# Optimization experiments

Hardware: AMD Instinct MI355X
Metric: run time of the kernel (lower is better)

## Reference

```python
import jax, jax.numpy as jnp
import numpy as np

DIM = 1024
HIDDEN = 4096
NUM_EXPERTS = 8
TOP_K = 2
B, S = 4, 2048


def setup_inputs() -> dict:
    key = jax.random.key(0)
    ks = jax.random.split(key, 5)
    scale_in = 1.0 / np.sqrt(DIM)
    scale_h = 1.0 / np.sqrt(HIDDEN)
    x = jax.random.normal(ks[0], (B, S, DIM), dtype=jnp.float32)
    gate_w = jax.random.normal(ks[1], (DIM, NUM_EXPERTS), dtype=jnp.float32) * scale_in
    w1 = jax.random.normal(ks[2], (NUM_EXPERTS, DIM, HIDDEN), dtype=jnp.float32) * scale_in
    w3 = jax.random.normal(ks[3], (NUM_EXPERTS, DIM, HIDDEN), dtype=jnp.float32) * scale_in
    w2 = jax.random.normal(ks[4], (NUM_EXPERTS, HIDDEN, DIM), dtype=jnp.float32) * scale_h
    return {"x": x, "gate_w": gate_w, "w1": w1, "w2": w2, "w3": w3}


def reference(x, gate_w, w1, w2, w3):
    b, s, d = x.shape
    e = w1.shape[0]
    k = TOP_K
    # --- Router ---
    gate_scores = jnp.einsum('bsd,de->bse', x, gate_w)           # [B,S,E]
    topk_vals, topk_idx = jax.lax.top_k(gate_scores, k)          # [B,S,K]
    topk_w = jax.nn.softmax(topk_vals, axis=-1)                  # [B,S,K]
    usage = jax.nn.softmax(gate_scores, axis=-1).mean(axis=(0, 1))  # [E]
    aux_loss = e * jnp.sum(usage ** 2)
    # --- Dispatch/combine weights: combine[t, e] = sum_k w where idx==e ---
    xf = x.reshape(-1, d)                                        # [T,D]
    idx_f = topk_idx.reshape(-1, k)                              # [T,K]
    w_f = topk_w.reshape(-1, k)                                  # [T,K]
    combine = jnp.sum(jax.nn.one_hot(idx_f, e, dtype=x.dtype) * w_f[..., None], axis=1)  # [T,E]
    # --- Per-expert SwiGLU, weighted combine (loop over fixed small E) ---
    out = jnp.zeros_like(xf)
    for ei in range(e):
        h = jax.nn.silu(xf @ w1[ei]) * (xf @ w3[ei])             # [T,H]
        y = h @ w2[ei]                                           # [T,D]
        out = out + combine[:, ei:ei + 1] * y
    return out.reshape(b, s, d), aux_loss
```

## Files before the change

### kernel.cpp

```cpp
#include <hip/hip_runtime.h>
#include <hip/hip_bf16.h>

#define NT 8192
#define DIM_ 1024
#define HID_ 4096
#define NE 8

#define TM 128
#define TN 128
#define BK 32

typedef unsigned short u16;
typedef __attribute__((ext_vector_type(8))) short bf16x8;
typedef __attribute__((ext_vector_type(4))) float f32x4;

__device__ __forceinline__ u16 f2b(float f) {
  unsigned u = __float_as_uint(f);
  return (u16)((u + 0x7FFFu + ((u >> 16) & 1u)) >> 16);
}

typedef __attribute__((address_space(1))) const unsigned int ga_u32;
typedef __attribute__((address_space(3))) unsigned int lds_u32;
__device__ __forceinline__ void gl16(const u16* g, u16* l) {
  __builtin_amdgcn_global_load_lds((ga_u32*)g, (lds_u32*)l, 16, 0, 0);
}

__global__ __launch_bounds__(256) void cvt_x_kernel(const float* __restrict__ x,
                                                    u16* __restrict__ xb) {
  int i = (blockIdx.x * 256 + threadIdx.x) * 4;
  f32x4 v = *(const f32x4*)(x + i);
  ushort4 o;
  o.x = f2b(v.x); o.y = f2b(v.y); o.z = f2b(v.z); o.w = f2b(v.w);
  *(ushort4*)(xb + i) = o;
}

__global__ __launch_bounds__(256) void tpose_kernel(const float* __restrict__ src,
                                                    u16* __restrict__ dst, int K, int N) {
  int e = blockIdx.z;
  int n0 = blockIdx.x * 64, k0 = blockIdx.y * 64;
  __shared__ u16 t[64][72];
  int tid = threadIdx.x;
  int kl = tid >> 4, cl = (tid & 15) * 4;
  const float* s = src + ((size_t)e * K + k0) * N + n0;
#pragma unroll
  for (int i = 0; i < 4; i++) {
    f32x4 v = *(const f32x4*)(s + (size_t)(kl + i * 16) * N + cl);
    ushort4 o; o.x = f2b(v.x); o.y = f2b(v.y); o.z = f2b(v.z); o.w = f2b(v.w);
    *(ushort4*)&t[kl + i * 16][cl] = o;
  }
  __syncthreads();
  int nl = tid >> 2, kc = (tid & 3) * 16;
  u16* d = dst + ((size_t)e * N + n0 + nl) * K + k0 + kc;
  unsigned p[8];
#pragma unroll
  for (int j = 0; j < 8; j++)
    p[j] = (unsigned)t[kc + 2 * j][nl] | ((unsigned)t[kc + 2 * j + 1][nl] << 16);
  *(uint4*)d = make_uint4(p[0], p[1], p[2], p[3]);
  *(uint4*)(d + 8) = make_uint4(p[4], p[5], p[6], p[7]);
}

__global__ __launch_bounds__(256) void router_kernel(
    const float* __restrict__ x, const float* __restrict__ gw,
    int* __restrict__ elist, float* __restrict__ pw,
    int* __restrict__ count, float* __restrict__ usage) {
  __shared__ float us[NE];
  int tid = threadIdx.x;
  if (tid < NE) us[tid] = 0.f;
  __syncthreads();
  int wave = tid >> 6, lane = tid & 63;
  int base = (blockIdx.x * 4 + wave) * 16;
  for (int i = 0; i < 16; ++i) {
    int t = base + i;
    float acc[NE];
#pragma unroll
    for (int e = 0; e < NE; e++) acc[e] = 0.f;
    for (int d = lane; d < DIM_; d += 64) {
      float xv = x[t * DIM_ + d];
      const float* g = gw + d * NE;
#pragma unroll
      for (int e = 0; e < NE; e++) acc[e] += xv * g[e];
    }
#pragma unroll
    for (int off = 32; off; off >>= 1) {
#pragma unroll
      for (int e = 0; e < NE; e++) acc[e] += __shfl_xor(acc[e], off);
    }
    if (lane == 0) {
      float m = acc[0];
#pragma unroll
      for (int e = 1; e < NE; e++) m = fmaxf(m, acc[e]);
      float Z = 0.f, ex[NE];
#pragma unroll
      for (int e = 0; e < NE; e++) { ex[e] = __expf(acc[e] - m); Z += ex[e]; }
#pragma unroll
      for (int e = 0; e < NE; e++) atomicAdd(&us[e], ex[e] / Z);
      int i0 = 0;
#pragma unroll
      for (int e = 1; e < NE; e++) if (acc[e] > acc[i0]) i0 = e;
      int i1 = -1;
#pragma unroll
      for (int e = 0; e < NE; e++) {
        if (e == i0) continue;
        if (i1 < 0 || acc[e] > acc[i1]) i1 = e;
      }
      float w0 = 1.f / (1.f + __expf(acc[i1] - acc[i0]));
      float w1 = 1.f - w0;
      int p0 = atomicAdd(&count[i0], 1);
      elist[i0 * NT + p0] = 2 * t;
      pw[2 * t] = w0;
      int p1 = atomicAdd(&count[i1], 1);
      elist[i1 * NT + p1] = 2 * t + 1;
      pw[2 * t + 1] = w1;
    }
  }
  __syncthreads();
  if (tid < NE) atomicAdd(&usage[tid], us[tid]);
}

__global__ void aux_kernel(const float* __restrict__ usage, float* __restrict__ out_aux) {
  if (threadIdx.x == 0) {
    float s = 0.f;
    for (int e = 0; e < NE; e++) { float u = usage[e] / (float)NT; s += u * u; }
    *out_aux = (float)NE * s;
  }
}

__global__ __launch_bounds__(256) void stage1_kernel(
    const u16* __restrict__ xb, const u16* __restrict__ wt1, const u16* __restrict__ wt3,
    const int* __restrict__ elist, const int* __restrict__ count,
    const float* __restrict__ pw, u16* __restrict__ hbuf) {
  int wgid = blockIdx.x;
  int e = wgid & 7;
  int k = wgid >> 3;
  int tile = k & 63;
  int n0 = (k >> 6) * TN;
  int cnt = count[e];
  if (tile * TM >= cnt) return;

  __shared__ u16 As[2][TM * BK];
  __shared__ u16 B1s[2][TN * BK];
  __shared__ u16 B3s[2][TN * BK];
  __shared__ int slots[TM];
  __shared__ float pws[TM];

  int tid = threadIdx.x;
  if (tid < TM) {
    int r = tile * TM + tid;
    int s = (r < cnt) ? elist[e * NT + r] : -1;
    slots[tid] = s;
    pws[tid] = (s >= 0) ? pw[s] : 0.f;
  }
  __syncthreads();

  int lrow = tid >> 2;
  int lcol = (tid & 3) * 8;
  int sl0 = slots[lrow], sl1 = slots[lrow + 64];
  const u16* gA0 = xb + (size_t)((sl0 >= 0 ? sl0 : 0) >> 1) * DIM_ + lcol;
  const u16* gA1 = xb + (size_t)((sl1 >= 0 ? sl1 : 0) >> 1) * DIM_ + lcol;
  const u16* gB1a = wt1 + ((size_t)e * HID_ + n0 + lrow) * DIM_ + lcol;
  const u16* gB1b = gB1a + (size_t)64 * DIM_;
  const u16* gB3a = wt3 + ((size_t)e * HID_ + n0 + lrow) * DIM_ + lcol;
  const u16* gB3b = gB3a + (size_t)64 * DIM_;

  int wv = tid >> 6, lane = tid & 63;
  int wm = (wv & 1) * 64, wn = (wv >> 1) * 64;
  int fr = lane & 15, fk = (lane >> 4) * 8;

  f32x4 acc1[4][4], acc3[4][4];
  f32x4 zero = {0.f, 0.f, 0.f, 0.f};
#pragma unroll
  for (int i = 0; i < 4; i++)
#pragma unroll
    for (int j = 0; j < 4; j++) { acc1[i][j] = zero; acc3[i][j] = zero; }

#define S1_STAGE(B, K0)                          \
  gl16(gA0 + (K0), &As[B][tid * 8]);             \
  gl16(gA1 + (K0), &As[B][2048 + tid * 8]);      \
  gl16(gB1a + (K0), &B1s[B][tid * 8]);           \
  gl16(gB1b + (K0), &B1s[B][2048 + tid * 8]);    \
  gl16(gB3a + (K0), &B3s[B][tid * 8]);           \
  gl16(gB3b + (K0), &B3s[B][2048 + tid * 8]);

#define S1_COMPUTE(B)                                                          \
  { bf16x8 afr[4], b1fr[4], b3fr[4];                                           \
    _Pragma("unroll") for (int i = 0; i < 4; i++)                              \
      afr[i] = *(const bf16x8*)&As[B][(wm + i * 16 + fr) * BK + fk];           \
    _Pragma("unroll") for (int j = 0; j < 4; j++) {                            \
      b1fr[j] = *(const bf16x8*)&B1s[B][(wn + j * 16 + fr) * BK + fk];         \
      b3fr[j] = *(const bf16x8*)&B3s[B][(wn + j * 16 + fr) * BK + fk];         \
    }                                                                          \
    _Pragma("unroll") for (int i = 0; i < 4; i++)                              \
      _Pragma("unroll") for (int j = 0; j < 4; j++) {                          \
        acc1[i][j] = __builtin_amdgcn_mfma_f32_16x16x32_bf16(afr[i], b1fr[j], acc1[i][j], 0, 0, 0); \
        acc3[i][j] = __builtin_amdgcn_mfma_f32_16x16x32_bf16(afr[i], b3fr[j], acc3[i][j], 0, 0, 0); \
      } }

  S1_STAGE(0, 0);
  __syncthreads();
  for (int k0 = 0; k0 < DIM_; k0 += 2 * BK) {
    S1_STAGE(1, k0 + BK);
    S1_COMPUTE(0);
    __syncthreads();
    if (k0 + 2 * BK < DIM_) { S1_STAGE(0, k0 + 2 * BK); }
    S1_COMPUTE(1);
    __syncthreads();
  }

#pragma unroll
  for (int i = 0; i < 4; i++) {
#pragma unroll
    for (int r4 = 0; r4 < 4; r4++) {
      int row = wm + i * 16 + (lane >> 4) * 4 + r4;
      int s = slots[row];
      if (s < 0) continue;
      float w = pws[row];
      u16* dst = hbuf + (size_t)s * HID_ + n0 + wn + (lane & 15);
#pragma unroll
      for (int j = 0; j < 4; j++) {
        float p1 = acc1[i][j][r4];
        float p3 = acc3[i][j][r4];
        float h = (p1 / (1.f + __expf(-p1))) * p3 * w;
        dst[j * 16] = f2b(h);
      }
    }
  }
}

__global__ __launch_bounds__(256) void stage2_kernel(
    const u16* __restrict__ hbuf, const u16* __restrict__ wt2,
    const int* __restrict__ elist, const int* __restrict__ count,
    float* __restrict__ out) {
  int wgid = blockIdx.x;
  int e = wgid & 7;
  int k = wgid >> 3;
  int tile = k & 63;
  int n0 = (k >> 6) * TN;
  int cnt = count[e];
  if (tile * TM >= cnt) return;

  __shared__ u16 As[2][TM * BK];
  __shared__ u16 Bs[2][TN * BK];
  __shared__ int slots[TM];

  int tid = threadIdx.x;
  if (tid < TM) {
    int r = tile * TM + tid;
    slots[tid] = (r < cnt) ? elist[e * NT + r] : -1;
  }
  __syncthreads();

  int lrow = tid >> 2;
  int lcol = (tid & 3) * 8;
  int sl0 = slots[lrow], sl1 = slots[lrow + 64];
  const u16* gA0 = hbuf + (size_t)(sl0 >= 0 ? sl0 : 0) * HID_ + lcol;
  const u16* gA1 = hbuf + (size_t)(sl1 >= 0 ? sl1 : 0) * HID_ + lcol;
  const u16* gBa = wt2 + ((size_t)e * DIM_ + n0 + lrow) * HID_ + lcol;
  const u16* gBb = gBa + (size_t)64 * HID_;

  int wv = tid >> 6, lane = tid & 63;
  int wm = (wv & 1) * 64, wn = (wv >> 1) * 64;
  int fr = lane & 15, fk = (lane >> 4) * 8;

  f32x4 acc[4][4];
  f32x4 zero = {0.f, 0.f, 0.f, 0.f};
#pragma unroll
  for (int i = 0; i < 4; i++)
#pragma unroll
    for (int j = 0; j < 4; j++) acc[i][j] = zero;

#define S2_STAGE(B, K0)                          \
  gl16(gA0 + (K0), &As[B][tid * 8]);             \
  gl16(gA1 + (K0), &As[B][2048 + tid * 8]);      \
  gl16(gBa + (K0), &Bs[B][tid * 8]);             \
  gl16(gBb + (K0), &Bs[B][2048 + tid * 8]);

#define S2_COMPUTE(B)                                                          \
  { bf16x8 afr[4], bfr[4];                                                     \
    _Pragma("unroll") for (int i = 0; i < 4; i++)                              \
      afr[i] = *(const bf16x8*)&As[B][(wm + i * 16 + fr) * BK + fk];           \
    _Pragma("unroll") for (int j = 0; j < 4; j++)                              \
      bfr[j] = *(const bf16x8*)&Bs[B][(wn + j * 16 + fr) * BK + fk];           \
    _Pragma("unroll") for (int i = 0; i < 4; i++)                              \
      _Pragma("unroll") for (int j = 0; j < 4; j++)                            \
        acc[i][j] = __builtin_amdgcn_mfma_f32_16x16x32_bf16(afr[i], bfr[j], acc[i][j], 0, 0, 0); }

  S2_STAGE(0, 0);
  __syncthreads();
  for (int k0 = 0; k0 < HID_; k0 += 2 * BK) {
    S2_STAGE(1, k0 + BK);
    S2_COMPUTE(0);
    __syncthreads();
    if (k0 + 2 * BK < HID_) { S2_STAGE(0, k0 + 2 * BK); }
    S2_COMPUTE(1);
    __syncthreads();
  }

#pragma unroll
  for (int i = 0; i < 4; i++) {
#pragma unroll
    for (int r4 = 0; r4 < 4; r4++) {
      int row = wm + i * 16 + (lane >> 4) * 4 + r4;
      int s = slots[row];
      if (s < 0) continue;
      int tk = s >> 1;
      float* dst = out + (size_t)tk * DIM_ + n0 + wn + (lane & 15);
#pragma unroll
      for (int j = 0; j < 4; j++) atomicAdd(&dst[j * 16], acc[i][j][r4]);
    }
  }
}

extern "C" void kernel_launch(void* const* d_in, const int* in_sizes, int n_in,
                              void* d_out, int out_size, void* d_ws, size_t ws_size,
                              hipStream_t stream) {
  const float* x = (const float*)d_in[0];
  const float* gw = (const float*)d_in[1];
  const float* w1 = (const float*)d_in[2];
  const float* w2 = (const float*)d_in[3];
  const float* w3 = (const float*)d_in[4];
  float* out = (float*)d_out;

  char* ws = (char*)d_ws;
  int* count = (int*)ws;
  float* usage = (float*)(ws + 32);
  int* elist = (int*)(ws + 256);
  float* pw = (float*)(ws + 256 + 262144);
  u16* xb = (u16*)(ws + 327936);
  u16* hbuf = (u16*)(ws + 327936 + 16777216);
  char* wbase = ws + 327936 + 16777216 + 134217728;
  u16* wt1 = (u16*)wbase;
  u16* wt3 = (u16*)(wbase + 67108864);
  u16* wt2 = (u16*)wbase;

  hipMemsetAsync(d_out, 0, (size_t)(NT * DIM_ + 1) * sizeof(float), stream);
  hipMemsetAsync(ws, 0, 64, stream);

  cvt_x_kernel<<<(NT * DIM_) / (256 * 4), 256, 0, stream>>>(x, xb);
  router_kernel<<<128, 256, 0, stream>>>(x, gw, elist, pw, count, usage);
  aux_kernel<<<1, 64, 0, stream>>>(usage, out + (size_t)NT * DIM_);
  tpose_kernel<<<dim3(HID_ / 64, DIM_ / 64, NE), 256, 0, stream>>>(w1, wt1, DIM_, HID_);
  tpose_kernel<<<dim3(HID_ / 64, DIM_ / 64, NE), 256, 0, stream>>>(w3, wt3, DIM_, HID_);
  stage1_kernel<<<dim3(NE * 64 * (HID_ / TN)), 256, 0, stream>>>(xb, wt1, wt3, elist, count, pw, hbuf);
  tpose_kernel<<<dim3(DIM_ / 64, HID_ / 64, NE), 256, 0, stream>>>(w2, wt2, HID_, DIM_);
  stage2_kernel<<<dim3(NE * 64 * (DIM_ / TN)), 256, 0, stream>>>(hbuf, wt2, elist, count, out);
}
```

Measured before the change: 1.604 ms.

## Triple-buffer LDS staging with vmcnt-based waits and one barrier per K step

Both GEMM stages move from a double-buffered loop with two __syncthreads per pair of K tiles to a three-stage ring of LDS buffers. Two tiles are kept in flight, and partial s_waitcnt vmcnt counts wait only for the oldest tile's global-to-LDS loads before a single barrier per step. The intent is deeper prefetch that hides global load latency and fewer full drains of outstanding memory operations. The cost is 50% more LDS per workgroup, which may lower occupancy. Correctness also depends on the hand-counted vmcnt values matching the number of loads issued per stage.

```diff
diff --git a/kernel.cpp b/kernel.cpp
--- a/kernel.cpp
+++ b/kernel.cpp
@@ -137,9 +137,9 @@
   int cnt = count[e];
   if (tile * TM >= cnt) return;
 
-  __shared__ u16 As[2][TM * BK];
-  __shared__ u16 B1s[2][TN * BK];
-  __shared__ u16 B3s[2][TN * BK];
+  __shared__ u16 As[3][TM * BK];
+  __shared__ u16 B1s[3][TN * BK];
+  __shared__ u16 B3s[3][TN * BK];
   __shared__ int slots[TM];
   __shared__ float pws[TM];
 
@@ -196,14 +196,22 @@
       } }
 
   S1_STAGE(0, 0);
-  __syncthreads();
-  for (int k0 = 0; k0 < DIM_; k0 += 2 * BK) {
-    S1_STAGE(1, k0 + BK);
-    S1_COMPUTE(0);
-    __syncthreads();
-    if (k0 + 2 * BK < DIM_) { S1_STAGE(0, k0 + 2 * BK); }
-    S1_COMPUTE(1);
-    __syncthreads();
+  S1_STAGE(1, BK);
+  int b0 = 0;
+  for (int k0 = 0; k0 < DIM_; k0 += BK) {
+    if (k0 + BK < DIM_) {
+      asm volatile("s_waitcnt vmcnt(6)" ::: "memory");
+    } else {
+      asm volatile("s_waitcnt vmcnt(0)" ::: "memory");
+    }
+    __builtin_amdgcn_s_barrier();
+    __builtin_amdgcn_sched_barrier(0);
+    if (k0 + 2 * BK < DIM_) {
+      int b2 = b0 + 2; if (b2 >= 3) b2 -= 3;
+      S1_STAGE(b2, k0 + 2 * BK);
+    }
+    S1_COMPUTE(b0);
+    if (++b0 == 3) b0 = 0;
   }
 
 #pragma unroll
@@ -238,8 +246,8 @@
   int cnt = count[e];
   if (tile * TM >= cnt) return;
 
-  __shared__ u16 As[2][TM * BK];
-  __shared__ u16 Bs[2][TN * BK];
+  __shared__ u16 As[3][TM * BK];
+  __shared__ u16 Bs[3][TN * BK];
   __shared__ int slots[TM];
 
   int tid = threadIdx.x;
@@ -285,14 +293,22 @@
         acc[i][j] = __builtin_amdgcn_mfma_f32_16x16x32_bf16(afr[i], bfr[j], acc[i][j], 0, 0, 0); }
 
   S2_STAGE(0, 0);
-  __syncthreads();
-  for (int k0 = 0; k0 < HID_; k0 += 2 * BK) {
-    S2_STAGE(1, k0 + BK);
-    S2_COMPUTE(0);
-    __syncthreads();
-    if (k0 + 2 * BK < HID_) { S2_STAGE(0, k0 + 2 * BK); }
-    S2_COMPUTE(1);
-    __syncthreads();
+  S2_STAGE(1, BK);
+  int b0 = 0;
+  for (int k0 = 0; k0 < HID_; k0 += BK) {
+    if (k0 + BK < HID_) {
+      asm volatile("s_waitcnt vmcnt(4)" ::: "memory");
+    } else {
+      asm volatile("s_waitcnt vmcnt(0)" ::: "memory");
+    }
+    __builtin_amdgcn_s_barrier();
+    __builtin_amdgcn_sched_barrier(0);
+    if (k0 + 2 * BK < HID_) {
+      int b2 = b0 + 2; if (b2 >= 3) b2 -= 3;
+      S2_STAGE(b2, k0 + 2 * BK);
+    }
+    S2_COMPUTE(b0);
+    if (++b0 == 3) b0 = 0;
   }
 
 #pragma unroll
```

After: 1.668 ms. 1.04x slower.

## Restructure stage1 GEMM into 256x128 tiles with swizzled LDS and interleaved pipeline

Applied to the files above, without the earlier changes.

Stage1 moves to 512 threads with 256-row, 64-deep K tiles and an XOR-swizzled LDS layout to avoid bank conflicts. The main loop is split into four sub-phases with explicit barriers, waitcnt and setprio, so global-to-LDS loads of the next buffer overlap MFMA work. The goal is more data reuse per tile and better hiding of memory latency. The cost is much larger LDS use and fragile hand-written synchronisation. The grid still covers 64 tiles per expert even though each tile now holds 256 rows, so many blocks exit early.

```diff
diff --git a/kernel.cpp b/kernel.cpp
--- a/kernel.cpp
+++ b/kernel.cpp
@@ -9,6 +9,10 @@
 #define TM 128
 #define TN 128
 #define BK 32
+
+#define TM1 256
+#define TN1 128
+#define BK1 64
 
 typedef unsigned short u16;
 typedef __attribute__((ext_vector_type(8))) short bf16x8;
@@ -125,7 +129,7 @@
   }
 }
 
-__global__ __launch_bounds__(256) void stage1_kernel(
+__global__ __launch_bounds__(512, 2) void stage1_kernel(
     const u16* __restrict__ xb, const u16* __restrict__ wt1, const u16* __restrict__ wt3,
     const int* __restrict__ elist, const int* __restrict__ count,
     const float* __restrict__ pw, u16* __restrict__ hbuf) {
@@ -133,38 +137,60 @@
   int e = wgid & 7;
   int k = wgid >> 3;
   int tile = k & 63;
-  int n0 = (k >> 6) * TN;
+  int n0 = (k >> 6) * TN1;
   int cnt = count[e];
-  if (tile * TM >= cnt) return;
-
-  __shared__ u16 As[2][TM * BK];
-  __shared__ u16 B1s[2][TN * BK];
-  __shared__ u16 B3s[2][TN * BK];
-  __shared__ int slots[TM];
-  __shared__ float pws[TM];
+  if (tile * TM1 >= cnt) return;
+
+  __shared__ u16 As[2][TM1 * BK1];
+  __shared__ u16 B1s[2][TN1 * BK1];
+  __shared__ u16 B3s[2][TN1 * BK1];
+  __shared__ int slots[TM1];
+  __shared__ float pws[TM1];
 
   int tid = threadIdx.x;
-  if (tid < TM) {
-    int r = tile * TM + tid;
+  if (tid < TM1) {
+    int r = tile * TM1 + tid;
     int s = (r < cnt) ? elist[e * NT + r] : -1;
     slots[tid] = s;
     pws[tid] = (s >= 0) ? pw[s] : 0.f;
   }
   __syncthreads();
 
-  int lrow = tid >> 2;
-  int lcol = (tid & 3) * 8;
-  int sl0 = slots[lrow], sl1 = slots[lrow + 64];
-  const u16* gA0 = xb + (size_t)((sl0 >= 0 ? sl0 : 0) >> 1) * DIM_ + lcol;
-  const u16* gA1 = xb + (size_t)((sl1 >= 0 ? sl1 : 0) >> 1) * DIM_ + lcol;
-  const u16* gB1a = wt1 + ((size_t)e * HID_ + n0 + lrow) * DIM_ + lcol;
-  const u16* gB1b = gB1a + (size_t)64 * DIM_;
-  const u16* gB3a = wt3 + ((size_t)e * HID_ + n0 + lrow) * DIM_ + lcol;
-  const u16* gB3b = gB3a + (size_t)64 * DIM_;
+  int srow = tid >> 3;
+  int scol = ((tid & 7) ^ (srow & 7)) * 8;
+  const u16* gA[2][2];
+#pragma unroll
+  for (int h = 0; h < 2; h++)
+#pragma unroll
+    for (int r = 0; r < 2; r++) {
+      int rr = h * 128 + r * 64 + srow;
+      int s = slots[rr];
+      gA[h][r] = xb + (size_t)((s >= 0 ? s : 0) >> 1) * DIM_ + scol;
+    }
+  const u16* gB1r0 = wt1 + ((size_t)e * HID_ + n0 + srow) * DIM_ + scol;
+  const u16* gB1r1 = gB1r0 + (size_t)64 * DIM_;
+  const u16* gB3r0 = wt3 + ((size_t)e * HID_ + n0 + srow) * DIM_ + scol;
+  const u16* gB3r1 = gB3r0 + (size_t)64 * DIM_;
+
+#define STG_A(BUF, H, K0)                                   \
+  gl16(gA[H][0] + (K0), &As[BUF][(H) * 8192 + tid * 8]);    \
+  gl16(gA[H][1] + (K0), &As[BUF][(H) * 8192 + 4096 + tid * 8]);
+#define STG_B1(BUF, K0)                                     \
+  gl16(gB1r0 + (K0), &B1s[BUF][tid * 8]);                   \
+  gl16(gB1r1 + (K0), &B1s[BUF][4096 + tid * 8]);
+#define STG_B3(BUF, K0)                                     \
+  gl16(gB3r0 + (K0), &B3s[BUF][tid * 8]);                   \
+  gl16(gB3r1 + (K0), &B3s[BUF][4096 + tid * 8]);
 
   int wv = tid >> 6, lane = tid & 63;
-  int wm = (wv & 1) * 64, wn = (wv >> 1) * 64;
-  int fr = lane & 15, fk = (lane >> 4) * 8;
+  int wm = (wv & 3) * 64;
+  int wn = (wv >> 2) * 64;
+  int fr = lane & 15, q = lane >> 4;
+  int sw = fr & 7;
+  int aof0 = (wm + fr) * 64 + ((q ^ sw)) * 8;
+  int aof1 = (wm + fr) * 64 + (((4 + q) ^ sw)) * 8;
+  int bof0 = (wn + fr) * 64 + ((q ^ sw)) * 8;
+  int bof1 = (wn + fr) * 64 + (((4 + q) ^ sw)) * 8;
 
   f32x4 acc1[4][4], acc3[4][4];
   f32x4 zero = {0.f, 0.f, 0.f, 0.f};
@@ -173,38 +199,67 @@
 #pragma unroll
     for (int j = 0; j < 4; j++) { acc1[i][j] = zero; acc3[i][j] = zero; }
 
-#define S1_STAGE(B, K0)                          \
-  gl16(gA0 + (K0), &As[B][tid * 8]);             \
-  gl16(gA1 + (K0), &As[B][2048 + tid * 8]);      \
-  gl16(gB1a + (K0), &B1s[B][tid * 8]);           \
-  gl16(gB1b + (K0), &B1s[B][2048 + tid * 8]);    \
-  gl16(gB3a + (K0), &B3s[B][tid * 8]);           \
-  gl16(gB3b + (K0), &B3s[B][2048 + tid * 8]);
-
-#define S1_COMPUTE(B)                                                          \
-  { bf16x8 afr[4], b1fr[4], b3fr[4];                                           \
+#define MM16(ACC, AF, BF)                                                      \
+  _Pragma("unroll") for (int i = 0; i < 4; i++)                                \
+    _Pragma("unroll") for (int j = 0; j < 4; j++)                              \
+      ACC[i][j] = __builtin_amdgcn_mfma_f32_16x16x32_bf16(AF[i], BF[j], ACC[i][j], 0, 0, 0);
+
+#define S1_ITER(CUR, NXT, KB, DO_STAGE, LASTV)                                 \
+  { bf16x8 a0[4], bb[4];                                                       \
     _Pragma("unroll") for (int i = 0; i < 4; i++)                              \
-      afr[i] = *(const bf16x8*)&As[B][(wm + i * 16 + fr) * BK + fk];           \
-    _Pragma("unroll") for (int j = 0; j < 4; j++) {                            \
-      b1fr[j] = *(const bf16x8*)&B1s[B][(wn + j * 16 + fr) * BK + fk];         \
-      b3fr[j] = *(const bf16x8*)&B3s[B][(wn + j * 16 + fr) * BK + fk];         \
-    }                                                                          \
+      a0[i] = *(const bf16x8*)&As[CUR][aof0 + i * 1024];                       \
+    _Pragma("unroll") for (int j = 0; j < 4; j++)                              \
+      bb[j] = *(const bf16x8*)&B1s[CUR][bof0 + j * 1024];                      \
+    if (DO_STAGE) { STG_A(NXT, 0, KB); }                                       \
+    __builtin_amdgcn_s_barrier();                                              \
+    asm volatile("s_waitcnt lgkmcnt(0)" ::: "memory");                         \
+    __builtin_amdgcn_sched_barrier(0);                                         \
+    __builtin_amdgcn_s_setprio(1); MM16(acc1, a0, bb); __builtin_amdgcn_s_setprio(0); \
+    asm volatile("s_waitcnt vmcnt(%0)" :: "i"((LASTV) ? 0 : 2) : "memory");    \
+    __builtin_amdgcn_s_barrier();                                              \
+                                                                       \
+    _Pragma("unroll") for (int j = 0; j < 4; j++)                              \
+      bb[j] = *(const bf16x8*)&B3s[CUR][bof0 + j * 1024];                      \
+    if (DO_STAGE) { STG_A(NXT, 1, KB); }                                       \
+    __builtin_amdgcn_s_barrier();                                              \
+    asm volatile("s_waitcnt lgkmcnt(0)" ::: "memory");                         \
+    __builtin_amdgcn_sched_barrier(0);                                         \
+    __builtin_amdgcn_s_setprio(1); MM16(acc3, a0, bb); __builtin_amdgcn_s_setprio(0); \
+    __builtin_amdgcn_s_barrier();                                              \
+                                                                       \
     _Pragma("unroll") for (int i = 0; i < 4; i++)                              \
-      _Pragma("unroll") for (int j = 0; j < 4; j++) {                          \
-        acc1[i][j] = __builtin_amdgcn_mfma_f32_16x16x32_bf16(afr[i], b1fr[j], acc1[i][j], 0, 0, 0); \
-        acc3[i][j] = __builtin_amdgcn_mfma_f32_16x16x32_bf16(afr[i], b3fr[j], acc3[i][j], 0, 0, 0); \
-      } }
-
-  S1_STAGE(0, 0);
-  __syncthreads();
-  for (int k0 = 0; k0 < DIM_; k0 += 2 * BK) {
-    S1_STAGE(1, k0 + BK);
-    S1_COMPUTE(0);
-    __syncthreads();
-    if (k0 + 2 * BK < DIM_) { S1_STAGE(0, k0 + 2 * BK); }
-    S1_COMPUTE(1);
-    __syncthreads();
-  }
+      a0[i] = *(const bf16x8*)&As[CUR][aof1 + i * 1024];                       \
+    _Pragma("unroll") for (int j = 0; j < 4; j++)                              \
+      bb[j] = *(const bf16x8*)&B1s[CUR][bof1 + j * 1024];                      \
+    if (DO_STAGE) { STG_B1(NXT, KB); }                                         \
+    __builtin_amdgcn_s_barrier();                                              \
+    asm volatile("s_waitcnt lgkmcnt(0)" ::: "memory");                         \
+    __builtin_amdgcn_sched_barrier(0);                                         \
+    __builtin_amdgcn_s_setprio(1); MM16(acc1, a0, bb); __builtin_amdgcn_s_setprio(0); \
+    __builtin_amdgcn_s_barrier();                                              \
+                                                                       \
+    _Pragma("unroll") for (int j = 0; j < 4; j++)                              \
+      bb[j] = *(const bf16x8*)&B3s[CUR][bof1 + j * 1024];                      \
+    if (DO_STAGE) { STG_B3(NXT, KB); }                                         \
+    __builtin_amdgcn_s_barrier();                                              \
+    asm volatile("s_waitcnt lgkmcnt(0)" ::: "memory");                         \
+    __builtin_amdgcn_sched_barrier(0);                                         \
+    __builtin_amdgcn_s_setprio(1); MM16(acc3, a0, bb); __builtin_amdgcn_s_setprio(0); \
+    if (DO_STAGE) { asm volatile("s_waitcnt vmcnt(2)" ::: "memory"); }         \
+    __builtin_amdgcn_s_barrier(); }
+
+  STG_A(0, 0, 0); STG_A(0, 1, 0); STG_B1(0, 0); STG_B3(0, 0);
+  asm volatile("s_waitcnt vmcnt(0)" ::: "memory");
+  __builtin_amdgcn_s_barrier();
+
+  for (int p = 0; p < 7; ++p) {
+    int kb1 = (2 * p + 1) * BK1;
+    int kb2 = (2 * p + 2) * BK1;
+    S1_ITER(0, 1, kb1, 1, 0);
+    S1_ITER(1, 0, kb2, 1, 0);
+  }
+  S1_ITER(0, 1, 15 * BK1, 1, 0);
+  S1_ITER(1, 0, 0, 0, 1);
 
 #pragma unroll
   for (int i = 0; i < 4; i++) {
@@ -238,8 +293,8 @@
   int cnt = count[e];
   if (tile * TM >= cnt) return;
 
-  __shared__ u16 As[2][TM * BK];
-  __shared__ u16 Bs[2][TN * BK];
+  __shared__ u16 As2[2][TM * BK];
+  __shared__ u16 Bs2[2][TN * BK];
   __shared__ int slots[TM];
 
   int tid = threadIdx.x;
@@ -269,17 +324,17 @@
     for (int j = 0; j < 4; j++) acc[i][j] = zero;
 
 #define S2_STAGE(B, K0)                          \
-  gl16(gA0 + (K0), &As[B][tid * 8]);             \
-  gl16(gA1 + (K0), &As[B][2048 + tid * 8]);      \
-  gl16(gBa + (K0), &Bs[B][tid * 8]);             \
-  gl16(gBb + (K0), &Bs[B][2048 + tid * 8]);
+  gl16(gA0 + (K0), &As2[B][tid * 8]);            \
+  gl16(gA1 + (K0), &As2[B][2048 + tid * 8]);     \
+  gl16(gBa + (K0), &Bs2[B][tid * 8]);            \
+  gl16(gBb + (K0), &Bs2[B][2048 + tid * 8]);
 
 #define S2_COMPUTE(B)                                                          \
   { bf16x8 afr[4], bfr[4];                                                     \
     _Pragma("unroll") for (int i = 0; i < 4; i++)                              \
-      afr[i] = *(const bf16x8*)&As[B][(wm + i * 16 + fr) * BK + fk];           \
-    _Pragma("unroll") for (int j = 0; j < 4; j++)                              \
-      bfr[j] = *(const bf16x8*)&Bs[B][(wn + j * 16 + fr) * BK + fk];           \
+      afr[i] = *(const bf16x8*)&As2[B][(wm + i * 16 + fr) * BK + fk];          \
+    _Pragma("unroll") for (int j = 0; j < 4; j++)                              \
+      bfr[j] = *(const bf16x8*)&Bs2[B][(wn + j * 16 + fr) * BK + fk];          \
     _Pragma("unroll") for (int i = 0; i < 4; i++)                              \
       _Pragma("unroll") for (int j = 0; j < 4; j++)                            \
         acc[i][j] = __builtin_amdgcn_mfma_f32_16x16x32_bf16(afr[i], bfr[j], acc[i][j], 0, 0, 0); }
@@ -340,7 +395,7 @@
   aux_kernel<<<1, 64, 0, stream>>>(usage, out + (size_t)NT * DIM_);
   tpose_kernel<<<dim3(HID_ / 64, DIM_ / 64, NE), 256, 0, stream>>>(w1, wt1, DIM_, HID_);
   tpose_kernel<<<dim3(HID_ / 64, DIM_ / 64, NE), 256, 0, stream>>>(w3, wt3, DIM_, HID_);
-  stage1_kernel<<<dim3(NE * 64 * (HID_ / TN)), 256, 0, stream>>>(xb, wt1, wt3, elist, count, pw, hbuf);
+  stage1_kernel<<<dim3(NE * 64 * (HID_ / TN1)), 512, 0, stream>>>(xb, wt1, wt3, elist, count, pw, hbuf);
   tpose_kernel<<<dim3(DIM_ / 64, HID_ / 64, NE), 256, 0, stream>>>(w2, wt2, HID_, DIM_);
   stage2_kernel<<<dim3(NE * 64 * (DIM_ / TN)), 256, 0, stream>>>(hbuf, wt2, elist, count, out);
 }
```

After: 1.312 ms. 18.2% less time.
